# Performance work log

Measured on AMD Instinct MI355X. Metric: run time of the kernel, lower is better.

## Reference

```python
import jax, jax.numpy as jnp
import numpy as np

B, T, S, L, R, H, UE = 64, 256, 16, 128, 16, 256, 64


def setup_inputs() -> dict:
    key = jax.random.key(0)
    ks = jax.random.split(key, 10)
    u = jax.random.normal(ks[0], (B, T, UE), jnp.float32)
    k = 0.1 * jax.random.normal(ks[1], (B, T, L), jnp.float32)
    K = 0.1 * jax.random.normal(ks[2], (B, T, L, R), jnp.float32)
    eps_z = jax.random.normal(ks[3], (T, S, B, L), jnp.float32)
    eps_w = jax.random.normal(ks[4], (T, S, B, R), jnp.float32)
    W1 = jax.random.normal(ks[5], (L, H), jnp.float32) / np.sqrt(L).astype(np.float32)
    W2 = jax.random.normal(ks[6], (H, L), jnp.float32) / np.sqrt(H).astype(np.float32)
    m_init = jax.random.normal(ks[7], (L,), jnp.float32)
    Q_diag = jax.random.uniform(ks[8], (L,), jnp.float32, 0.1, 1.0)
    Q0_diag = jax.random.uniform(ks[9], (L,), jnp.float32, 0.5, 1.5)
    return dict(u=u, k=k, K=K, eps_z=eps_z, eps_w=eps_w, W1=W1, W2=W2,
                m_init=m_init, Q_diag=Q_diag, Q0_diag=Q0_diag, n_samples=S)


def reference(u, k, K, eps_z, eps_w, W1, W2, m_init, Q_diag, Q0_diag, n_samples):
    Bn, Tn, Ln, Rn = K.shape
    ue = u.shape[-1]
    I_r = jnp.eye(Rn, dtype=K.dtype)

    def bmv(A, x):      # A: [B,L,R], x: [...,B,R] -> [...,B,L]
        return jnp.einsum('blr,...br->...bl', A, x)

    def bmvT(A, x):     # A: [B,L,R], x: [...,B,L] -> [...,B,R]
        return jnp.einsum('blr,...bl->...br', A, x)

    def mean_fn(z):
        return z + jnp.tanh(z @ W1) @ W2

    def step_core(m, K_t, k_t, ez, ew, q_a):
        # A = I + K^T diag(q_a) K  (rank x rank)
        A = I_r + jnp.einsum('blr,l,blq->brq', K_t, q_a, K_t)
        Lc = jnp.linalg.cholesky(A)
        Linv = jax.scipy.linalg.solve_triangular(
            Lc, jnp.broadcast_to(I_r, Lc.shape), lower=True)

        def csolve(x):  # solve A y = x via Linv^T Linv x
            y = jnp.einsum('bij,...bj->...bi', Linv, x)
            return jnp.einsum('bji,...bj->...bi', Linv, y)

        # gain direction; inner shift always uses Q_diag (as in torch source)
        g = k_t - bmv(K_t, csolve(bmvT(K_t, m + Q_diag * k_t)))
        m_f = m + q_a * g
        z_p = jnp.sqrt(q_a) * ez
        z_f = m_f + z_p - bmv(K_t, csolve(bmvT(K_t, z_p) + ew))
        qp = jnp.sum(q_a * g * g, axis=-1)
        M = A - I_r  # = K^T diag(q_a) K
        tr = -jnp.einsum('bij,bjk,bik->b', Linv, M, Linv)
        logdet = 2.0 * jnp.sum(jnp.log(jnp.diagonal(Lc, axis1=-2, axis2=-1)), axis=-1)
        kl = 0.5 * (qp + tr + logdet)
        return z_f, m_f, z_p, kl

    # ---- t = 0 (uses initial covariance Q0_diag) ----
    m0 = jnp.broadcast_to(m_init, (Bn, Ln))
    m0 = m0.at[:, :ue].add(u[:, 0])
    z_f0, m_f0, z_p0, kl0 = step_core(m0, K[:, 0], k[:, 0], eps_z[0], eps_w[0], Q0_diag)

    # ---- t = 1..T-1: sequential nonlinear filter scan ----
    def scan_fn(z_prev, xs):
        u_t, k_t, K_t, ez, ew = xs
        m = mean_fn(z_prev)            # [S,B,L]
        m = m.at[..., :ue].add(u_t)    # broadcast input over samples
        z_f, m_f, z_p, kl = step_core(m, K_t, k_t, ez, ew, Q_diag)
        return z_f, (z_f, m_f.mean(axis=0), z_p, kl.mean(axis=0))

    xs = (jnp.swapaxes(u[:, 1:], 0, 1),
          jnp.swapaxes(k[:, 1:], 0, 1),
          jnp.swapaxes(K[:, 1:], 0, 1),
          eps_z[1:], eps_w[1:])
    _, (z_fs, m_fs, z_ps, kls) = jax.lax.scan(scan_fn, z_f0, xs)

    z_f = jnp.transpose(jnp.concatenate([z_f0[None], z_fs], 0), (1, 2, 0, 3))  # [S,B,T,L]
    m_f = jnp.transpose(jnp.concatenate([m_f0[None], m_fs], 0), (1, 0, 2))     # [B,T,L]
    z_p = jnp.transpose(jnp.concatenate([z_p0[None], z_ps], 0), (1, 2, 0, 3))  # [S,B,T,L]
    kl = jnp.concatenate([kl0[None], kls], 0).T                                 # [B,T]
    return z_f, m_f, z_p, kl
```

## Files before the change

### kernel.cpp

```cpp
#include <hip/hip_runtime.h>
#include <cstddef>

typedef _Float16 half8v __attribute__((ext_vector_type(8)));
typedef _Float16 half4v __attribute__((ext_vector_type(4)));
typedef float f32x4 __attribute__((ext_vector_type(4)));

#define MFMA32(A, B, C) __builtin_amdgcn_mfma_f32_16x16x32_f16(A, B, C, 0, 0, 0)
#define MFMA16(A, B, C) __builtin_amdgcn_mfma_f32_16x16x16f16(A, B, C, 0, 0, 0)

__global__ void kw2_kernel(const float* __restrict__ W2, _Float16* __restrict__ w2h) {
  int i = blockIdx.x * 256 + threadIdx.x;
  w2h[i] = (_Float16)W2[i];
}

__global__ void kprep1_kernel(const float* __restrict__ Kg,
                              const float* __restrict__ kg,
                              const float* __restrict__ ug,
                              const float* __restrict__ Qd,
                              const float* __restrict__ Q0d,
                              float* __restrict__ Ainv,
                              float* __restrict__ klc,
                              _Float16* __restrict__ pfb,
                              float* __restrict__ cgp) {
  int tid = threadIdx.x;
  int wv = tid >> 6, ln = tid & 63;
  size_t bt = (size_t)blockIdx.x * 4 + wv;
  int t = (int)(bt & 255);
  __shared__ float Ks[4][128][20];
  __shared__ float qs[4][128];
  __shared__ float vvs[4][128];
  __shared__ float Asm[4][16][20];
  __shared__ float LiL[4][16][20];
  __shared__ float AiS[4][16][20];
  __shared__ float yps[4][4][16];
  __shared__ float yvs[4][16];

  const float* kp = Kg + bt * 2048;
  for (int i = ln; i < 2048; i += 64) Ks[wv][i >> 4][i & 15] = kp[i];
  for (int l = ln; l < 128; l += 64) {
    float q = (t == 0) ? Q0d[l] : Qd[l];
    qs[wv][l] = q;
    float v = Qd[l] * kg[bt * 128 + l];
    if (t > 0 && l < 64) v += ug[bt * 64 + l];
    vvs[wv][l] = v;
  }
  __syncthreads();
  {
    int r = ln & 15, c0 = (ln >> 4) << 2;
    float a0 = 0, a1 = 0, a2 = 0, a3 = 0;
    for (int l = 0; l < 128; ++l) {
      float kq = Ks[wv][l][r] * qs[wv][l];
      const float* row = &Ks[wv][l][c0];
      a0 += kq * row[0]; a1 += kq * row[1]; a2 += kq * row[2]; a3 += kq * row[3];
    }
    Asm[wv][r][c0 + 0] = a0 + ((r == c0 + 0) ? 1.f : 0.f);
    Asm[wv][r][c0 + 1] = a1 + ((r == c0 + 1) ? 1.f : 0.f);
    Asm[wv][r][c0 + 2] = a2 + ((r == c0 + 2) ? 1.f : 0.f);
    Asm[wv][r][c0 + 3] = a3 + ((r == c0 + 3) ? 1.f : 0.f);
  }
  {
    int r = ln & 15, seg = ln >> 4;
    float s = 0.f;
    for (int l = seg * 32; l < seg * 32 + 32; ++l) s += Ks[wv][l][r] * vvs[wv][l];
    yps[wv][seg][r] = s;
  }
  __syncthreads();
  if (ln < 16) {
    int i = ln;
    float ar[16], Lr[16];
#pragma unroll
    for (int j = 0; j < 16; ++j) ar[j] = Asm[wv][i][j];
    float ld = 0.f;
#pragma unroll
    for (int j = 0; j < 16; ++j) {
      float ajj = __shfl(ar[j], j, 64);
      float d = sqrtf(ajj);
      ld += __logf(d);
      float li = ar[j] / d;
      li = (i >= j) ? li : 0.f;
      Lr[j] = li;
#pragma unroll
      for (int k2 = j; k2 < 16; ++k2) {
        float lk = __shfl(li, k2, 64);
        ar[k2] -= li * lk;
      }
    }
    int cc = i;
    float Lic[16];
#pragma unroll
    for (int ii = 0; ii < 16; ++ii) {
      float s = (ii == cc) ? 1.f : 0.f;
#pragma unroll
      for (int p = 0; p < 16; ++p) {
        if (p < ii) {
          float Lip = __shfl(Lr[p], ii, 64);
          s -= Lip * Lic[p];
        }
      }
      float dii = __shfl(Lr[ii], ii, 64);
      float v = s / dii;
      Lic[ii] = (ii >= cc) ? v : 0.f;
    }
    float tr = 0.f;
#pragma unroll
    for (int ii = 0; ii < 16; ++ii) { tr += Lic[ii] * Lic[ii]; LiL[wv][cc][ii] = Lic[ii]; }
    tr += __shfl_xor(tr, 1); tr += __shfl_xor(tr, 2);
    tr += __shfl_xor(tr, 4); tr += __shfl_xor(tr, 8);
    if (cc == 0) klc[bt] = 0.5f * (tr - 16.f + 2.f * ld);
    yvs[wv][cc] = yps[wv][0][cc] + yps[wv][1][cc] + yps[wv][2][cc] + yps[wv][3][cc];
  }
  __syncthreads();
  {
    int r = ln & 15, c0 = (ln >> 4) << 2;
    float a0 = 0, a1 = 0, a2 = 0, a3 = 0;
    for (int ii = 0; ii < 16; ++ii) {
      float lir = LiL[wv][r][ii];
      a0 += lir * LiL[wv][c0 + 0][ii];
      a1 += lir * LiL[wv][c0 + 1][ii];
      a2 += lir * LiL[wv][c0 + 2][ii];
      a3 += lir * LiL[wv][c0 + 3][ii];
    }
    AiS[wv][r][c0 + 0] = a0; AiS[wv][r][c0 + 1] = a1;
    AiS[wv][r][c0 + 2] = a2; AiS[wv][r][c0 + 3] = a3;
    f32x4 av = {a0, a1, a2, a3};
    *(f32x4*)&Ainv[bt * 256 + r * 16 + c0] = av;
  }
  __syncthreads();
  {
#pragma unroll
    for (int li = 0; li < 2; ++li) {
      int l = ln * 2 + li;
      f32x4 acc0 = {0,0,0,0}, acc1v = {0,0,0,0}, acc2v = {0,0,0,0}, acc3v = {0,0,0,0};
      for (int j = 0; j < 16; ++j) {
        float kj = Ks[wv][l][j];
        acc0  += kj * *(const f32x4*)&AiS[wv][j][0];
        acc1v += kj * *(const f32x4*)&AiS[wv][j][4];
        acc2v += kj * *(const f32x4*)&AiS[wv][j][8];
        acc3v += kj * *(const f32x4*)&AiS[wv][j][12];
      }
      float ql = qs[wv][l];
      float cp = ql * kg[bt * 128 + l];
      float pv[16];
#pragma unroll
      for (int e = 0; e < 4; ++e) {
        pv[e] = ql * acc0[e]; pv[4 + e] = ql * acc1v[e];
        pv[8 + e] = ql * acc2v[e]; pv[12 + e] = ql * acc3v[e];
      }
#pragma unroll
      for (int r = 0; r < 16; ++r) cp -= pv[r] * yvs[wv][r];
      cgp[bt * 128 + l] = cp;
#pragma unroll
      for (int r = 0; r < 16; ++r) Ks[wv][l][r] = pv[r];
    }
  }
  __syncthreads();
  {
    int gp = ln >> 4, cp = ln & 15;
#pragma unroll
    for (int ci = 0; ci < 4; ++ci) {
      half8v o;
#pragma unroll
      for (int mt = 0; mt < 2; ++mt)
#pragma unroll
        for (int j = 0; j < 4; ++j)
          o[mt * 4 + j] = (_Float16)Ks[wv][ci * 32 + mt * 16 + cp][gp * 4 + j];
      *(half8v*)(pfb + bt * 2048 + (size_t)(ci * 64 + ln) * 8) = o;
    }
  }
}

__global__ void kprepR_kernel(const float* __restrict__ Kg,
                              const _Float16* __restrict__ w2h,
                              _Float16* __restrict__ rfb,
                              _Float16* __restrict__ kab) {
  int tid = threadIdx.x;
  int wv = tid >> 6, ln = tid & 63;
  int g = ln >> 4, c = ln & 15;
  __shared__ _Float16 Kh[128][20];
  __shared__ _Float16 Rh[16][264];
  for (int it = 0; it < 4; ++it) {
    size_t bt = (size_t)blockIdx.x * 4 + it;
    const float* kp = Kg + bt * 2048;
    for (int i = tid; i < 2048; i += 256) Kh[i >> 4][i & 15] = (_Float16)kp[i];
    __syncthreads();
    half8v kA[4];
#pragma unroll
    for (int kt = 0; kt < 4; ++kt)
#pragma unroll
      for (int j = 0; j < 8; ++j) kA[kt][j] = Kh[kt * 32 + g * 8 + j][c];
#pragma unroll
    for (int i = 0; i < 4; ++i) {
      int tile = wv * 4 + i;
      f32x4 acc = {0, 0, 0, 0};
#pragma unroll
      for (int kt = 0; kt < 4; ++kt) {
        half8v bf = *(const half8v*)&w2h[(size_t)(tile * 16 + c) * 128 + kt * 32 + g * 8];
        acc = MFMA32(kA[kt], bf, acc);
      }
#pragma unroll
      for (int r = 0; r < 4; ++r) Rh[g * 4 + r][tile * 16 + c] = (_Float16)acc[r];
    }
    __syncthreads();
    half8v r0, r1;
#pragma unroll
    for (int mt = 0; mt < 4; ++mt)
#pragma unroll
      for (int j = 0; j < 4; ++j) {
        _Float16 v = Rh[c][wv * 64 + mt * 16 + g * 4 + j];
        if (mt < 2) r0[mt * 4 + j] = v; else r1[(mt - 2) * 4 + j] = v;
      }
    *(half8v*)(rfb + bt * 4096 + (size_t)tid * 16) = r0;
    *(half8v*)(rfb + bt * 4096 + (size_t)tid * 16 + 8) = r1;
    if (kab) {
      half8v ko;
#pragma unroll
      for (int kt = 0; kt < 2; ++kt)
#pragma unroll
        for (int j = 0; j < 4; ++j) ko[kt * 4 + j] = Kh[wv * 32 + kt * 16 + g * 4 + j][c];
      *(half8v*)(kab + bt * 2048 + (size_t)tid * 8) = ko;
    }
    __syncthreads();
  }
}

__global__ void kc_kernel(const float* __restrict__ Kg,
                          const float* __restrict__ epsz,
                          const float* __restrict__ epsw,
                          const float* __restrict__ Qd,
                          const float* __restrict__ Q0d,
                          const float* __restrict__ Ainv,
                          float* __restrict__ out_zf,
                          float* __restrict__ out_zp,
                          float* __restrict__ zpcb,
                          int zw, int wzp) {
  int idx = blockIdx.x;
  int t = idx >> 6, b = idx & 63;
  int bt = b * 256 + t;
  __shared__ float Ks[128][16];
  __shared__ float Ai[16][16];
  __shared__ float zp[16][129];
  __shared__ float hh[16][17];
  __shared__ float ww[16][17];
  __shared__ float sq[128];
  const float* kp = Kg + (size_t)bt * 2048;
  for (int i = threadIdx.x; i < 2048; i += 256) ((float*)Ks)[i] = kp[i];
  ((float*)Ai)[threadIdx.x] = Ainv[(size_t)bt * 256 + threadIdx.x];
  const float* q = (t == 0) ? Q0d : Qd;
  if (threadIdx.x < 128) sq[threadIdx.x] = sqrtf(q[threadIdx.x]);
  __syncthreads();
  for (int i = threadIdx.x; i < 2048; i += 256) {
    int s = i >> 7, l = i & 127;
    float v = sq[l] * epsz[(((size_t)t * 16 + s) * 64 + b) * 128 + l];
    zp[s][l] = v;
    if (wzp) out_zp[(((size_t)s * 64 + b) * 256 + t) * 128 + l] = v;
  }
  __syncthreads();
  {
    int s = threadIdx.x >> 4, r = threadIdx.x & 15;
    float acc = epsw[(((size_t)t * 16 + s) * 64 + b) * 16 + r];
    for (int l = 0; l < 128; ++l) acc += Ks[l][r] * zp[s][l];
    hh[s][r] = acc;
  }
  __syncthreads();
  {
    int s = threadIdx.x >> 4, r = threadIdx.x & 15;
    float acc = 0.f;
    for (int j = 0; j < 16; ++j) acc += Ai[r][j] * hh[s][j];
    ww[s][r] = acc;
  }
  __syncthreads();
  for (int i = threadIdx.x; i < 2048; i += 256) {
    int s = i >> 7, l = i & 127;
    float acc = 0.f;
    for (int r = 0; r < 16; ++r) acc += Ks[l][r] * ww[s][r];
    float v = zp[s][l] - acc;
    if (zw) zpcb[(size_t)bt * 2048 + i] = v;
    else out_zf[(((size_t)s * 64 + b) * 256 + t) * 128 + l] = v;
  }
}

__global__ void kzp_kernel(const float* __restrict__ epsz,
                           const float* __restrict__ Qd,
                           const float* __restrict__ Q0d,
                           float* __restrict__ out_zp) {
  for (size_t i = (size_t)blockIdx.x * blockDim.x + threadIdx.x; i < (size_t)33554432;
       i += (size_t)gridDim.x * blockDim.x) {
    int l = (int)(i & 127);
    int t = (int)((i >> 7) & 255);
    int sb = (int)(i >> 15);
    int s = sb >> 6, b = sb & 63;
    float q = (t == 0) ? Q0d[l] : Qd[l];
    out_zp[i] = sqrtf(q) * epsz[(((size_t)t * 16 + s) * 64 + b) * 128 + l];
  }
}

#define BAR() asm volatile("s_waitcnt lgkmcnt(0)\n\ts_barrier" ::: "memory")

template <bool PK, bool ZW>
__device__ __forceinline__ void scan_body(
    const int b, const int ct,
    _Float16* __restrict__ svhc, _Float16* __restrict__ hbc,
    float (*__restrict__ h2pc)[320], float (*__restrict__ qppc)[64],
    const float* __restrict__ ug, const float* __restrict__ Kg,
    const float* __restrict__ W1, const float* __restrict__ W2,
    const float* __restrict__ m_init, const float* __restrict__ Qd,
    const float* __restrict__ Q0d, const _Float16* __restrict__ pfb,
    const float* __restrict__ cgp, const _Float16* __restrict__ rfb,
    const _Float16* __restrict__ kab, const float* __restrict__ zpcb,
    const float* __restrict__ klcp, float* __restrict__ out_zf,
    float* __restrict__ out_mf, float* __restrict__ out_kl) {
  const int wvc = ct >> 6;
  const int ln = ct & 63;
  const int g = ln >> 4;
  const int c = ln & 15;

  half8v w1f[4][4];
#pragma unroll
  for (int mt = 0; mt < 4; ++mt)
#pragma unroll
    for (int kt = 0; kt < 4; ++kt) {
      half8v v;
#pragma unroll
      for (int j = 0; j < 8; ++j)
        v[j] = (_Float16)W1[(size_t)(kt * 32 + g * 8 + j) * 256 + (wvc * 64 + mt * 16 + c)];
      w1f[mt][kt] = v;
    }
  half8v w2f[2][8];
#pragma unroll
  for (int mt = 0; mt < 2; ++mt)
#pragma unroll
    for (int kt = 0; kt < 8; ++kt) {
      half8v v;
#pragma unroll
      for (int j = 0; j < 8; ++j)
        v[j] = (_Float16)W2[(size_t)(kt * 32 + g * 8 + j) * 128 + (wvc * 32 + mt * 16 + c)];
      w2f[mt][kt] = v;
    }

  f32x4 qiv[2], qiv0[2];
#pragma unroll
  for (int mt = 0; mt < 2; ++mt) {
    f32x4 q = *(const f32x4*)&Qd[wvc * 32 + mt * 16 + g * 4];
    f32x4 q0 = *(const f32x4*)&Q0d[wvc * 32 + mt * 16 + g * 4];
#pragma unroll
    for (int r = 0; r < 4; ++r) { qiv[mt][r] = 1.f / q[r]; qiv0[mt][r] = 1.f / q0[r]; }
  }

  f32x4 zreg[2];

  half8v pfx0, pfx1, kax0 = {}, kax1 = {}, rfa0, rfa1, rfc0, rfc1;
  float kf0[8], kf1[8];
  f32x4 zq0[2], zq1[2], cv0[2], cv1[2];
  f32x4 ur0[2] = {}, ur1[2] = {};
  float kv0 = 0.f, kv1 = 0.f;

  const char* pf_p = (const char*)pfb + (size_t)b * 256 * 4096 + (size_t)ct * 16;
  const char* ka_p = PK ? (const char*)kab + (size_t)b * 256 * 4096 + (size_t)ct * 16
                        : (const char*)pfb;
  const char* K_p = (const char*)Kg + (size_t)b * 256 * 8192 + (size_t)((wvc * 32 + g * 4) * 16 + c) * 4;
  const char* rf_p = (const char*)rfb + (size_t)b * 256 * 8192 + (size_t)ct * 32;
  const char* zq_p = ZW ? (const char*)zpcb + (size_t)b * 256 * 8192 + (size_t)(c * 128 + wvc * 32 + g * 4) * 4
                        : (const char*)out_zf + ((((size_t)c * 64 + b) * 256) * 128 + wvc * 32 + g * 4) * 4;
  const size_t zq_str = ZW ? 8192 : 512;
  const char* cv_p = (const char*)cgp + (size_t)b * 256 * 512 + (size_t)(wvc * 32 + g * 4) * 4;
  const char* ur_p = (const char*)ug + (size_t)b * 256 * 256 + (size_t)(wvc * 32 + g * 4) * 4;
  const char* kl_p = (const char*)klcp + (size_t)b * 256 * 4;
  char* zf_p = (char*)out_zf + ((((size_t)c * 64 + b) * 256) * 128 + wvc * 32 + g * 4) * 4;
  char* mf_p = (char*)out_mf + ((size_t)b * 256 * 128 + wvc * 32 + g * 4) * 4;

#define STAGE(BI) do { \
    pfx##BI = *(const half8v*)pf_p; pf_p += 4096; \
    if constexpr (PK) { kax##BI = *(const half8v*)ka_p; ka_p += 4096; } \
    else { _Pragma("unroll") for (int kt_ = 0; kt_ < 2; ++kt_) \
             _Pragma("unroll") for (int j_ = 0; j_ < 4; ++j_) \
               kf##BI[kt_ * 4 + j_] = *(const float*)(K_p + kt_ * 1024 + j_ * 64); \
           K_p += 8192; } \
    rfa##BI = *(const half8v*)rf_p; rfc##BI = *(const half8v*)(rf_p + 16); rf_p += 8192; \
    zq##BI[0] = *(const f32x4*)zq_p; zq##BI[1] = *(const f32x4*)(zq_p + 64); zq_p += zq_str; \
    cv##BI[0] = *(const f32x4*)cv_p; cv##BI[1] = *(const f32x4*)(cv_p + 64); cv_p += 512; \
    if (wvc < 2) { ur##BI[0] = *(const f32x4*)ur_p; ur##BI[1] = *(const f32x4*)(ur_p + 64); } \
    ur_p += 256; \
    kv##BI = *(const float*)kl_p; kl_p += 4; \
  } while (0)

#define KAH(BI, KT, DST) do { \
    if constexpr (PK) { _Pragma("unroll") for (int j_ = 0; j_ < 4; ++j_) DST[j_] = kax##BI[(KT) * 4 + j_]; } \
    else { _Pragma("unroll") for (int j_ = 0; j_ < 4; ++j_) DST[j_] = (_Float16)kf##BI[(KT) * 4 + j_]; } \
  } while (0)

#define PHASE_A(BI) do { \
    half4v zbh_[2], zbl_[2]; \
    _Pragma("unroll") for (int kt = 0; kt < 2; ++kt) \
      _Pragma("unroll") for (int j = 0; j < 4; ++j) { \
        float x_ = zreg[kt][j]; _Float16 h_ = (_Float16)x_; \
        zbh_[kt][j] = h_; zbl_[kt][j] = (_Float16)(x_ - (float)h_); } \
    half8v zh8_[4]; \
    _Pragma("unroll") for (int kt = 0; kt < 4; ++kt) { \
      int row_ = kt * 4 + g; \
      int idx_ = row_ * 128 + (((c + row_) & 15) << 3); \
      zh8_[kt] = *(const half8v*)&svhc[idx_]; } \
    f32x4 a1h_[4]; \
    _Pragma("unroll") for (int mt = 0; mt < 4; ++mt) a1h_[mt] = (f32x4){0,0,0,0}; \
    _Pragma("unroll") for (int kt = 0; kt < 4; ++kt) \
      _Pragma("unroll") for (int mt = 0; mt < 4; ++mt) \
        a1h_[mt] = MFMA32(w1f[mt][kt], zh8_[kt], a1h_[mt]); \
    half4v th_[4]; \
    _Pragma("unroll") for (int mt = 0; mt < 4; ++mt) { \
      _Pragma("unroll") for (int r = 0; r < 4; ++r) { \
        float x_ = a1h_[mt][r]; \
        float e_ = __expf(2.f * x_); \
        th_[mt][r] = (_Float16)(1.f - 2.f / (e_ + 1.f)); } \
      int row_ = wvc * 8 + mt * 2 + (g >> 1); \
      *(half4v*)&hbc[row_ * 128 + (((c + row_) & 15) << 3) + ((g & 1) << 2)] = th_[mt]; } \
    half4v ka0_, ka1_; KAH(BI, 0, ka0_); KAH(BI, 1, ka1_); \
    f32x4 hz_ = {0, 0, 0, 0}; \
    hz_ = MFMA16(ka0_, zbh_[0], hz_); hz_ = MFMA16(ka1_, zbh_[1], hz_); \
    hz_ = MFMA16(ka0_, zbl_[0], hz_); hz_ = MFMA16(ka1_, zbl_[1], hz_); \
    f32x4 hr_ = {0, 0, 0, 0}; \
    _Pragma("unroll") for (int mt = 0; mt < 4; ++mt) { \
      half4v rr_; \
      _Pragma("unroll") for (int j = 0; j < 4; ++j) \
        rr_[j] = (mt < 2) ? rfa##BI[mt * 4 + j] : rfc##BI[(mt - 2) * 4 + j]; \
      hr_ = MFMA16(rr_, th_[mt], hr_); } \
    *(f32x4*)&h2pc[wvc][c * 20 + g * 4] = hz_ + hr_; \
  } while (0)

#define EPILOG(BI, QIV, MV) do { \
    f32x4 h2v_ = *(const f32x4*)&h2pc[0][c * 20 + g * 4]; \
    h2v_ += *(const f32x4*)&h2pc[1][c * 20 + g * 4]; \
    h2v_ += *(const f32x4*)&h2pc[2][c * 20 + g * 4]; \
    h2v_ += *(const f32x4*)&h2pc[3][c * 20 + g * 4]; \
    half4v h2h_, h2l_; \
    _Pragma("unroll") for (int j = 0; j < 4; ++j) { \
      _Float16 h_ = (_Float16)h2v_[j]; \
      h2h_[j] = h_; h2l_[j] = (_Float16)(h2v_[j] - (float)h_); } \
    float qpl_ = 0.f; \
    _Pragma("unroll") for (int mt = 0; mt < 2; ++mt) { \
      half4v pfm_; \
      _Pragma("unroll") for (int j = 0; j < 4; ++j) pfm_[j] = pfx##BI[mt * 4 + j]; \
      f32x4 zz_ = {0, 0, 0, 0}; \
      f32x4 mh_ = MFMA16(pfm_, h2h_, zz_); \
      f32x4 mlv_ = MFMA16(pfm_, h2l_, zz_); \
      f32x4 dd_ = cv##BI[mt] - (mh_ + mlv_); \
      f32x4 mf_ = MV[mt] + dd_; \
      f32x4 zf_ = mf_ + zq##BI[mt]; \
      _Pragma("unroll") for (int r = 0; r < 4; ++r) qpl_ += dd_[r] * dd_[r] * QIV[mt][r]; \
      *(f32x4*)(zf_p + mt * 64) = zf_; \
      zreg[mt] = zf_; \
      half4v zh4_; \
      _Pragma("unroll") for (int r = 0; r < 4; ++r) zh4_[r] = (_Float16)zf_[r]; \
      int row_ = wvc * 4 + mt * 2 + (g >> 1); \
      int base_ = row_ * 128 + (((c + row_) & 15) << 3) + ((g & 1) << 2); \
      *(half4v*)&svhc[base_] = zh4_; \
      f32x4 ms_ = mf_; \
      _Pragma("unroll") for (int r = 0; r < 4; ++r) { \
        float x_ = ms_[r]; \
        x_ += __shfl_xor(x_, 1); x_ += __shfl_xor(x_, 2); \
        x_ += __shfl_xor(x_, 4); x_ += __shfl_xor(x_, 8); \
        ms_[r] = x_ * 0.0625f; } \
      if (c == 0) *(f32x4*)(mf_p + mt * 64) = ms_; \
    } \
    zf_p += 512; mf_p += 512; \
    qpl_ += __shfl_xor(qpl_, 16); \
    qpl_ += __shfl_xor(qpl_, 32); \
    if (g == 0) qppc[BI][wvc * 16 + c] = qpl_; \
  } while (0)

#define PHASE_B(BI, QIV) do { \
    half8v hf_[8]; \
    _Pragma("unroll") for (int kt = 0; kt < 8; ++kt) { \
      int row_ = kt * 4 + g; \
      hf_[kt] = *(const half8v*)&hbc[row_ * 128 + (((c + row_) & 15) << 3)]; } \
    f32x4 a2a_[2], a2b_[2]; \
    _Pragma("unroll") for (int mt = 0; mt < 2; ++mt) { a2a_[mt] = (f32x4){0,0,0,0}; a2b_[mt] = (f32x4){0,0,0,0}; } \
    _Pragma("unroll") for (int kt = 0; kt < 4; ++kt) \
      _Pragma("unroll") for (int mt = 0; mt < 2; ++mt) { \
        a2a_[mt] = MFMA32(w2f[mt][kt], hf_[kt], a2a_[mt]); \
        a2b_[mt] = MFMA32(w2f[mt][kt + 4], hf_[kt + 4], a2b_[mt]); } \
    f32x4 mv_[2]; \
    _Pragma("unroll") for (int mt = 0; mt < 2; ++mt) { \
      mv_[mt] = zreg[mt] + a2a_[mt] + a2b_[mt]; \
      if (wvc < 2) mv_[mt] += ur##BI[mt]; } \
    EPILOG(BI, QIV, mv_); \
  } while (0)

#define KL_FIN(PBI, TPREV) do { \
    if (ct < 16) { \
      float v_ = qppc[PBI][ct] + qppc[PBI][16 + ct] + qppc[PBI][32 + ct] + qppc[PBI][48 + ct]; \
      v_ += __shfl_xor(v_, 1); v_ += __shfl_xor(v_, 2); \
      v_ += __shfl_xor(v_, 4); v_ += __shfl_xor(v_, 8); \
      if (ct == 0) out_kl[(size_t)b * 256 + (size_t)(TPREV)] = 0.03125f * v_ + kv##PBI; \
    } \
  } while (0)

  STAGE(0);
  STAGE(1);
  {
    f32x4 mv0[2];
#pragma unroll
    for (int mt = 0; mt < 2; ++mt) {
      mv0[mt] = *(const f32x4*)&m_init[wvc * 32 + mt * 16 + g * 4];
      if (wvc < 2) mv0[mt] += ur0[mt];
    }
    half4v mh0[2], ml0[2];
#pragma unroll
    for (int kt = 0; kt < 2; ++kt)
#pragma unroll
      for (int j = 0; j < 4; ++j) {
        float x = mv0[kt][j];
        _Float16 h = (_Float16)x;
        mh0[kt][j] = h;
        ml0[kt][j] = (_Float16)(x - (float)h);
      }
    half4v ka0_, ka1_;
    KAH(0, 0, ka0_); KAH(0, 1, ka1_);
    f32x4 hz = {0, 0, 0, 0};
    hz = MFMA16(ka0_, mh0[0], hz); hz = MFMA16(ka1_, mh0[1], hz);
    hz = MFMA16(ka0_, ml0[0], hz); hz = MFMA16(ka1_, ml0[1], hz);
    *(f32x4*)&h2pc[wvc][c * 20 + g * 4] = hz;
    BAR();
    EPILOG(0, qiv0, mv0);
    BAR();
  }

  for (int t = 1; t < 255; t += 2) {
    KL_FIN(0, t - 1);
    STAGE(0);
    PHASE_A(1);
    BAR();
    PHASE_B(1, qiv);
    BAR();
    KL_FIN(1, t);
    STAGE(1);
    PHASE_A(0);
    BAR();
    PHASE_B(0, qiv);
    BAR();
  }
  KL_FIN(0, 254);
  PHASE_A(1);
  BAR();
  PHASE_B(1, qiv);
  BAR();
  KL_FIN(1, 255);

#undef STAGE
#undef KAH
#undef PHASE_A
#undef EPILOG
#undef PHASE_B
#undef KL_FIN
}

template <bool PK, bool ZW>
__launch_bounds__(256, 1)
__global__ void kscan1_kernel(const float* __restrict__ ug, const float* __restrict__ Kg,
                              const float* __restrict__ W1, const float* __restrict__ W2,
                              const float* __restrict__ m_init, const float* __restrict__ Qd,
                              const float* __restrict__ Q0d, const _Float16* __restrict__ pfb,
                              const float* __restrict__ cgp, const _Float16* __restrict__ rfb,
                              const _Float16* __restrict__ kab, const float* __restrict__ zpcb,
                              const float* __restrict__ klcp, float* __restrict__ out_zf,
                              float* __restrict__ out_mf, float* __restrict__ out_kl) {
  __shared__ __align__(16) _Float16 svh[2048];
  __shared__ __align__(16) _Float16 hb[4096];
  __shared__ float h2p[4][320];
  __shared__ float qpp[2][64];
  scan_body<PK, ZW>(blockIdx.x, threadIdx.x, svh, hb, h2p, qpp,
                    ug, Kg, W1, W2, m_init, Qd, Q0d, pfb, cgp, rfb, kab, zpcb, klcp,
                    out_zf, out_mf, out_kl);
}

template <bool PK, bool ZW>
__attribute__((amdgpu_flat_work_group_size(512, 512)))
__attribute__((amdgpu_waves_per_eu(2, 2)))
__global__ void kscan2_kernel(const float* __restrict__ ug, const float* __restrict__ Kg,
                              const float* __restrict__ W1, const float* __restrict__ W2,
                              const float* __restrict__ m_init, const float* __restrict__ Qd,
                              const float* __restrict__ Q0d, const _Float16* __restrict__ pfb,
                              const float* __restrict__ cgp, const _Float16* __restrict__ rfb,
                              const _Float16* __restrict__ kab, const float* __restrict__ zpcb,
                              const float* __restrict__ klcp, float* __restrict__ out_zf,
                              float* __restrict__ out_mf, float* __restrict__ out_kl) {
  __shared__ __align__(16) _Float16 svh[2][2048];
  __shared__ __align__(16) _Float16 hb[2][4096];
  __shared__ float h2p[2][4][320];
  __shared__ float qpp[2][2][64];
  const int ch = threadIdx.x >> 8;
  scan_body<PK, ZW>(blockIdx.x * 2 + ch, threadIdx.x & 255,
                    svh[ch], hb[ch], h2p[ch], qpp[ch],
                    ug, Kg, W1, W2, m_init, Qd, Q0d, pfb, cgp, rfb, kab, zpcb, klcp,
                    out_zf, out_mf, out_kl);
}

extern "C" void kernel_launch(void* const* d_in, const int* in_sizes, int n_in,
                              void* d_out, int out_size, void* d_ws, size_t ws_size,
                              hipStream_t stream) {
  (void)in_sizes; (void)n_in; (void)out_size;
  const float* u   = (const float*)d_in[0];
  const float* kk  = (const float*)d_in[1];
  const float* Kg  = (const float*)d_in[2];
  const float* epz = (const float*)d_in[3];
  const float* epw = (const float*)d_in[4];
  const float* W1  = (const float*)d_in[5];
  const float* W2  = (const float*)d_in[6];
  const float* mi  = (const float*)d_in[7];
  const float* Qd  = (const float*)d_in[8];
  const float* Q0d = (const float*)d_in[9];

  float* out_zf = (float*)d_out;
  float* out_mf = out_zf + (size_t)33554432;
  float* out_zp = out_mf + (size_t)2097152;
  float* out_kl = out_zp + (size_t)33554432;

  char* ws = (char*)d_ws;
  size_t off = 0;
  auto take = [&](size_t n) { char* p = ws + off; off += n; return p; };
  float*    Ainv = (float*)take(16777216);
  float*    klc  = (float*)take(65536);
  float*    cgp  = (float*)take(8388608);
  _Float16* pfb  = (_Float16*)take(67108864);
  _Float16* w2h  = (_Float16*)take(65536);
  bool zw = ws_size >= off + 134217728;
  float* zpcb = zw ? (float*)take(134217728) : nullptr;
  bool pk = zw && (ws_size >= off + 67108864);
  _Float16* kab = pk ? (_Float16*)take(67108864) : nullptr;
  bool rfws = ws_size >= off + 134217728;
  _Float16* rfb = rfws ? (_Float16*)take(134217728) : (_Float16*)out_zp;
  int wzp = rfws ? 1 : 0;

  kw2_kernel<<<128, 256, 0, stream>>>(W2, w2h);
  kprep1_kernel<<<4096, 256, 0, stream>>>(Kg, kk, u, Qd, Q0d, Ainv, klc, pfb, cgp);
  kprepR_kernel<<<4096, 256, 0, stream>>>(Kg, w2h, rfb, kab);
  kc_kernel<<<16384, 256, 0, stream>>>(Kg, epz, epw, Qd, Q0d, Ainv, out_zf, out_zp,
                                       zpcb, zw ? 1 : 0, wzp);

  auto pick = [&](const void* f2) {
    hipFuncAttributes fa;
    if (hipFuncGetAttributes(&fa, f2) == hipSuccess)
      return fa.localSizeBytes == 0 && fa.numRegs > 140;
    return false;
  };
#define LAUNCH_SCAN(PKV, ZWV) do { \
    if (pick((const void*)kscan2_kernel<PKV, ZWV>)) \
      kscan2_kernel<PKV, ZWV><<<32, 512, 0, stream>>>(u, Kg, W1, W2, mi, Qd, Q0d, pfb, cgp, rfb, kab, zpcb, klc, out_zf, out_mf, out_kl); \
    else \
      kscan1_kernel<PKV, ZWV><<<64, 256, 0, stream>>>(u, Kg, W1, W2, mi, Qd, Q0d, pfb, cgp, rfb, kab, zpcb, klc, out_zf, out_mf, out_kl); \
  } while (0)

  if (pk)      LAUNCH_SCAN(true,  true);
  else if (zw) LAUNCH_SCAN(false, true);
  else         LAUNCH_SCAN(false, false);
#undef LAUNCH_SCAN

  if (!rfws) kzp_kernel<<<2048, 256, 0, stream>>>(epz, Qd, Q0d, out_zp);
}
```

Baseline: 1.078 ms.

## Interleave two batch chains per 256-thread block in scan kernel

Replaces the 512-thread two-chain scan kernel with a 256-thread kernel in which each wave processes two independent batch elements (A and B), interleaving their phases so one chain's MFMA and memory latency can hide behind the other's. W1/W2 fragments are held in registers across both chains, and the launch picker now only requires zero scratch spills. This gives more instruction-level parallelism per wave at the cost of much higher register pressure, and it uses half as many waves per block.

```diff
diff --git a/kernel.cpp b/kernel.cpp
--- a/kernel.cpp
+++ b/kernel.cpp
@@ -572,9 +572,8 @@
 }
 
 template <bool PK, bool ZW>
-__attribute__((amdgpu_flat_work_group_size(512, 512)))
-__attribute__((amdgpu_waves_per_eu(2, 2)))
-__global__ void kscan2_kernel(const float* __restrict__ ug, const float* __restrict__ Kg,
+__launch_bounds__(256, 1)
+__global__ void kscand_kernel(const float* __restrict__ ug, const float* __restrict__ Kg,
                               const float* __restrict__ W1, const float* __restrict__ W2,
                               const float* __restrict__ m_init, const float* __restrict__ Qd,
                               const float* __restrict__ Q0d, const _Float16* __restrict__ pfb,
@@ -582,15 +581,293 @@
                               const _Float16* __restrict__ kab, const float* __restrict__ zpcb,
                               const float* __restrict__ klcp, float* __restrict__ out_zf,
                               float* __restrict__ out_mf, float* __restrict__ out_kl) {
+  const int tid = threadIdx.x;
+  const int wvc = tid >> 6;
+  const int ln = tid & 63;
+  const int g = ln >> 4;
+  const int c = ln & 15;
+  const int bA = blockIdx.x * 2;
+  const int bB = bA + 1;
+
   __shared__ __align__(16) _Float16 svh[2][2048];
   __shared__ __align__(16) _Float16 hb[2][4096];
   __shared__ float h2p[2][4][320];
   __shared__ float qpp[2][2][64];
-  const int ch = threadIdx.x >> 8;
-  scan_body<PK, ZW>(blockIdx.x * 2 + ch, threadIdx.x & 255,
-                    svh[ch], hb[ch], h2p[ch], qpp[ch],
-                    ug, Kg, W1, W2, m_init, Qd, Q0d, pfb, cgp, rfb, kab, zpcb, klcp,
-                    out_zf, out_mf, out_kl);
+
+  half8v w1f[4][4];
+#pragma unroll
+  for (int mt = 0; mt < 4; ++mt)
+#pragma unroll
+    for (int kt = 0; kt < 4; ++kt) {
+      half8v v;
+#pragma unroll
+      for (int j = 0; j < 8; ++j)
+        v[j] = (_Float16)W1[(size_t)(kt * 32 + g * 8 + j) * 256 + (wvc * 64 + mt * 16 + c)];
+      w1f[mt][kt] = v;
+    }
+  half8v w2f[2][8];
+#pragma unroll
+  for (int mt = 0; mt < 2; ++mt)
+#pragma unroll
+    for (int kt = 0; kt < 8; ++kt) {
+      half8v v;
+#pragma unroll
+      for (int j = 0; j < 8; ++j)
+        v[j] = (_Float16)W2[(size_t)(kt * 32 + g * 8 + j) * 128 + (wvc * 32 + mt * 16 + c)];
+      w2f[mt][kt] = v;
+    }
+
+  f32x4 qiv[2];
+#pragma unroll
+  for (int mt = 0; mt < 2; ++mt) {
+    f32x4 q = *(const f32x4*)&Qd[wvc * 32 + mt * 16 + g * 4];
+#pragma unroll
+    for (int r = 0; r < 4; ++r) qiv[mt][r] = 1.f / q[r];
+  }
+
+  f32x4 zregA[2], zregB[2];
+  half8v pfxA, pfxB, kaxA = {}, kaxB = {}, rfaA, rfaB, rfcA, rfcB;
+  float kfA[8], kfB[8];
+  f32x4 zqA[2], zqB[2], cvA[2], cvB[2], urA[2] = {}, urB[2] = {};
+  float kvA = 0.f, kvB = 0.f;
+
+  const int lo16 = tid * 16;
+  const int lo32 = tid * 32;
+  const int loK = ((wvc * 32 + g * 4) * 16 + c) * 4;
+  const int lodim = (wvc * 32 + g * 4) * 4;
+  const size_t zqlane = (size_t)(c * 128 + wvc * 32 + g * 4) * 4;
+  const size_t zflane = (size_t)c * 8388608 + (size_t)lodim;
+
+#define DSTAGE1(CH, BT) do { \
+    size_t o_ = (size_t)(BT); \
+    pfx##CH = *(const half8v*)((const char*)pfb + o_ * 4096 + lo16); \
+    if constexpr (PK) { kax##CH = *(const half8v*)((const char*)kab + o_ * 4096 + lo16); } \
+    else { _Pragma("unroll") for (int kt_ = 0; kt_ < 2; ++kt_) \
+             _Pragma("unroll") for (int j_ = 0; j_ < 4; ++j_) \
+               kf##CH[kt_ * 4 + j_] = *(const float*)((const char*)Kg + o_ * 8192 + loK + kt_ * 1024 + j_ * 64); } \
+    rfa##CH = *(const half8v*)((const char*)rfb + o_ * 8192 + lo32); \
+    rfc##CH = *(const half8v*)((const char*)rfb + o_ * 8192 + lo32 + 16); \
+  } while (0)
+
+#define DSTAGE2(CH, B_, BT, T) do { \
+    size_t o_ = (size_t)(BT); \
+    if constexpr (ZW) { \
+      zq##CH[0] = *(const f32x4*)((const char*)zpcb + o_ * 8192 + zqlane); \
+      zq##CH[1] = *(const f32x4*)((const char*)zpcb + o_ * 8192 + zqlane + 64); \
+    } else { \
+      size_t zo_ = (size_t)(B_) * 131072 + (size_t)(T) * 512 + zflane; \
+      zq##CH[0] = *(const f32x4*)((const char*)out_zf + zo_); \
+      zq##CH[1] = *(const f32x4*)((const char*)out_zf + zo_ + 64); \
+    } \
+    cv##CH[0] = *(const f32x4*)((const char*)cgp + o_ * 512 + lodim); \
+    cv##CH[1] = *(const f32x4*)((const char*)cgp + o_ * 512 + lodim + 64); \
+    if (wvc < 2) { \
+      ur##CH[0] = *(const f32x4*)((const char*)ug + o_ * 256 + lodim); \
+      ur##CH[1] = *(const f32x4*)((const char*)ug + o_ * 256 + lodim + 64); \
+    } \
+    kv##CH = klcp[BT]; \
+  } while (0)
+
+#define DKAH(CH, KT, DST) do { \
+    if constexpr (PK) { _Pragma("unroll") for (int j_ = 0; j_ < 4; ++j_) DST[j_] = kax##CH[(KT) * 4 + j_]; } \
+    else { _Pragma("unroll") for (int j_ = 0; j_ < 4; ++j_) DST[j_] = (_Float16)kf##CH[(KT) * 4 + j_]; } \
+  } while (0)
+
+#define DPHA(CH, CHI) do { \
+    half4v zbh_[2], zbl_[2]; \
+    _Pragma("unroll") for (int kt = 0; kt < 2; ++kt) \
+      _Pragma("unroll") for (int j = 0; j < 4; ++j) { \
+        float x_ = zreg##CH[kt][j]; _Float16 h_ = (_Float16)x_; \
+        zbh_[kt][j] = h_; zbl_[kt][j] = (_Float16)(x_ - (float)h_); } \
+    half8v zh8_[4]; \
+    _Pragma("unroll") for (int kt = 0; kt < 4; ++kt) { \
+      int row_ = kt * 4 + g; \
+      zh8_[kt] = *(const half8v*)&svh[CHI][row_ * 128 + (((c + row_) & 15) << 3)]; } \
+    f32x4 a1a_[4], a1b_[4]; \
+    _Pragma("unroll") for (int mt = 0; mt < 4; ++mt) { a1a_[mt] = (f32x4){0,0,0,0}; a1b_[mt] = (f32x4){0,0,0,0}; } \
+    _Pragma("unroll") for (int mt = 0; mt < 4; ++mt) { \
+      a1a_[mt] = MFMA32(w1f[mt][0], zh8_[0], a1a_[mt]); \
+      a1a_[mt] = MFMA32(w1f[mt][1], zh8_[1], a1a_[mt]); \
+      a1b_[mt] = MFMA32(w1f[mt][2], zh8_[2], a1b_[mt]); \
+      a1b_[mt] = MFMA32(w1f[mt][3], zh8_[3], a1b_[mt]); } \
+    half4v th_[4]; \
+    _Pragma("unroll") for (int mt = 0; mt < 4; ++mt) { \
+      _Pragma("unroll") for (int r = 0; r < 4; ++r) { \
+        float x_ = a1a_[mt][r] + a1b_[mt][r]; \
+        float e_ = __expf(2.f * x_); \
+        th_[mt][r] = (_Float16)(1.f - 2.f / (e_ + 1.f)); } \
+      int row_ = wvc * 8 + mt * 2 + (g >> 1); \
+      *(half4v*)&hb[CHI][row_ * 128 + (((c + row_) & 15) << 3) + ((g & 1) << 2)] = th_[mt]; } \
+    half4v ka0_, ka1_; DKAH(CH, 0, ka0_); DKAH(CH, 1, ka1_); \
+    f32x4 hz_ = {0, 0, 0, 0}; \
+    hz_ = MFMA16(ka0_, zbh_[0], hz_); hz_ = MFMA16(ka1_, zbh_[1], hz_); \
+    hz_ = MFMA16(ka0_, zbl_[0], hz_); hz_ = MFMA16(ka1_, zbl_[1], hz_); \
+    f32x4 hr_ = {0, 0, 0, 0}; \
+    _Pragma("unroll") for (int mt = 0; mt < 4; ++mt) { \
+      half4v rr_; \
+      _Pragma("unroll") for (int j = 0; j < 4; ++j) \
+        rr_[j] = (mt < 2) ? rfa##CH[mt * 4 + j] : rfc##CH[(mt - 2) * 4 + j]; \
+      hr_ = MFMA16(rr_, th_[mt], hr_); } \
+    *(f32x4*)&h2p[CHI][wvc][c * 20 + g * 4] = hz_ + hr_; \
+  } while (0)
+
+#define DEPI(CH, CHI, B_, T, QIV, MV) do { \
+    f32x4 h2v_ = *(const f32x4*)&h2p[CHI][0][c * 20 + g * 4]; \
+    h2v_ += *(const f32x4*)&h2p[CHI][1][c * 20 + g * 4]; \
+    h2v_ += *(const f32x4*)&h2p[CHI][2][c * 20 + g * 4]; \
+    h2v_ += *(const f32x4*)&h2p[CHI][3][c * 20 + g * 4]; \
+    half4v h2h_, h2l_; \
+    _Pragma("unroll") for (int j = 0; j < 4; ++j) { \
+      _Float16 h_ = (_Float16)h2v_[j]; \
+      h2h_[j] = h_; h2l_[j] = (_Float16)(h2v_[j] - (float)h_); } \
+    float qpl_ = 0.f; \
+    _Pragma("unroll") for (int mt = 0; mt < 2; ++mt) { \
+      half4v pfm_; \
+      _Pragma("unroll") for (int j = 0; j < 4; ++j) pfm_[j] = pfx##CH[mt * 4 + j]; \
+      f32x4 zz_ = {0, 0, 0, 0}; \
+      f32x4 mh_ = MFMA16(pfm_, h2h_, zz_); \
+      f32x4 mlv_ = MFMA16(pfm_, h2l_, zz_); \
+      f32x4 dd_ = cv##CH[mt] - (mh_ + mlv_); \
+      f32x4 mf_ = MV[mt] + dd_; \
+      f32x4 zf_ = mf_ + zq##CH[mt]; \
+      _Pragma("unroll") for (int r = 0; r < 4; ++r) qpl_ += dd_[r] * dd_[r] * QIV[mt][r]; \
+      *(f32x4*)((char*)out_zf + (size_t)(B_) * 131072 + (size_t)(T) * 512 + zflane + mt * 64) = zf_; \
+      zreg##CH[mt] = zf_; \
+      half4v zh4_; \
+      _Pragma("unroll") for (int r = 0; r < 4; ++r) zh4_[r] = (_Float16)zf_[r]; \
+      int row_ = wvc * 4 + mt * 2 + (g >> 1); \
+      *(half4v*)&svh[CHI][row_ * 128 + (((c + row_) & 15) << 3) + ((g & 1) << 2)] = zh4_; \
+      f32x4 ms_ = mf_; \
+      _Pragma("unroll") for (int r = 0; r < 4; ++r) { \
+        float x_ = ms_[r]; \
+        x_ += __shfl_xor(x_, 1); x_ += __shfl_xor(x_, 2); \
+        x_ += __shfl_xor(x_, 4); x_ += __shfl_xor(x_, 8); \
+        ms_[r] = x_ * 0.0625f; } \
+      if (c == 0) \
+        *(f32x4*)((char*)out_mf + ((size_t)(B_) * 256 + (size_t)(T)) * 512 + lodim + mt * 64) = ms_; \
+    } \
+    qpl_ += __shfl_xor(qpl_, 16); \
+    qpl_ += __shfl_xor(qpl_, 32); \
+    if (g == 0) qpp[CHI][(T) & 1][wvc * 16 + c] = qpl_; \
+  } while (0)
+
+#define DPHB(CH, CHI, B_, T, QIV) do { \
+    half8v hfa_[4]; \
+    _Pragma("unroll") for (int kt = 0; kt < 4; ++kt) { \
+      int row_ = kt * 4 + g; \
+      hfa_[kt] = *(const half8v*)&hb[CHI][row_ * 128 + (((c + row_) & 15) << 3)]; } \
+    f32x4 a2a_[2]; \
+    a2a_[0] = (f32x4){0,0,0,0}; a2a_[1] = (f32x4){0,0,0,0}; \
+    _Pragma("unroll") for (int kt = 0; kt < 4; ++kt) \
+      _Pragma("unroll") for (int mt = 0; mt < 2; ++mt) \
+        a2a_[mt] = MFMA32(w2f[mt][kt], hfa_[kt], a2a_[mt]); \
+    half8v hfb_[4]; \
+    _Pragma("unroll") for (int kt = 0; kt < 4; ++kt) { \
+      int row_ = (kt + 4) * 4 + g; \
+      hfb_[kt] = *(const half8v*)&hb[CHI][row_ * 128 + (((c + row_) & 15) << 3)]; } \
+    f32x4 a2b_[2]; \
+    a2b_[0] = (f32x4){0,0,0,0}; a2b_[1] = (f32x4){0,0,0,0}; \
+    _Pragma("unroll") for (int kt = 0; kt < 4; ++kt) \
+      _Pragma("unroll") for (int mt = 0; mt < 2; ++mt) \
+        a2b_[mt] = MFMA32(w2f[mt][kt + 4], hfb_[kt], a2b_[mt]); \
+    f32x4 mv_[2]; \
+    _Pragma("unroll") for (int mt = 0; mt < 2; ++mt) { \
+      mv_[mt] = zreg##CH[mt] + a2a_[mt] + a2b_[mt]; \
+      if (wvc < 2) mv_[mt] += ur##CH[mt]; } \
+    DEPI(CH, CHI, B_, T, QIV, mv_); \
+  } while (0)
+
+#define DKL(CH, CHI, B_, TPREV) do { \
+    if (tid < 16) { \
+      const float* qq_ = qpp[CHI][(TPREV) & 1]; \
+      float v_ = qq_[tid] + qq_[16 + tid] + qq_[32 + tid] + qq_[48 + tid]; \
+      v_ += __shfl_xor(v_, 1); v_ += __shfl_xor(v_, 2); \
+      v_ += __shfl_xor(v_, 4); v_ += __shfl_xor(v_, 8); \
+      if (tid == 0) out_kl[(size_t)(B_) * 256 + (size_t)(TPREV)] = 0.03125f * v_ + kv##CH; \
+    } \
+  } while (0)
+
+  {
+    int btA = bA * 256, btB = bB * 256;
+    DSTAGE1(A, btA); DSTAGE1(B, btB);
+    DSTAGE2(A, bA, btA, 0); DSTAGE2(B, bB, btB, 0);
+    f32x4 qiv0[2];
+#pragma unroll
+    for (int mt = 0; mt < 2; ++mt) {
+      f32x4 q0 = *(const f32x4*)&Q0d[wvc * 32 + mt * 16 + g * 4];
+#pragma unroll
+      for (int r = 0; r < 4; ++r) qiv0[mt][r] = 1.f / q0[r];
+    }
+    f32x4 mvA_[2], mvB_[2];
+#pragma unroll
+    for (int mt = 0; mt < 2; ++mt) {
+      f32x4 mi = *(const f32x4*)&m_init[wvc * 32 + mt * 16 + g * 4];
+      mvA_[mt] = mi; mvB_[mt] = mi;
+      if (wvc < 2) { mvA_[mt] += urA[mt]; mvB_[mt] += urB[mt]; }
+    }
+    {
+      half4v mh0[2], ml0[2];
+#pragma unroll
+      for (int kt = 0; kt < 2; ++kt)
+#pragma unroll
+        for (int j = 0; j < 4; ++j) {
+          float x = mvA_[kt][j];
+          _Float16 h = (_Float16)x;
+          mh0[kt][j] = h; ml0[kt][j] = (_Float16)(x - (float)h);
+        }
+      half4v ka0_, ka1_;
+      DKAH(A, 0, ka0_); DKAH(A, 1, ka1_);
+      f32x4 hz = {0, 0, 0, 0};
+      hz = MFMA16(ka0_, mh0[0], hz); hz = MFMA16(ka1_, mh0[1], hz);
+      hz = MFMA16(ka0_, ml0[0], hz); hz = MFMA16(ka1_, ml0[1], hz);
+      *(f32x4*)&h2p[0][wvc][c * 20 + g * 4] = hz;
+    }
+    {
+      half4v mh0[2], ml0[2];
+#pragma unroll
+      for (int kt = 0; kt < 2; ++kt)
+#pragma unroll
+        for (int j = 0; j < 4; ++j) {
+          float x = mvB_[kt][j];
+          _Float16 h = (_Float16)x;
+          mh0[kt][j] = h; ml0[kt][j] = (_Float16)(x - (float)h);
+        }
+      half4v ka0_, ka1_;
+      DKAH(B, 0, ka0_); DKAH(B, 1, ka1_);
+      f32x4 hz = {0, 0, 0, 0};
+      hz = MFMA16(ka0_, mh0[0], hz); hz = MFMA16(ka1_, mh0[1], hz);
+      hz = MFMA16(ka0_, ml0[0], hz); hz = MFMA16(ka1_, ml0[1], hz);
+      *(f32x4*)&h2p[1][wvc][c * 20 + g * 4] = hz;
+    }
+    BAR();
+    DEPI(A, 0, bA, 0, qiv0, mvA_);
+    DEPI(B, 1, bB, 0, qiv0, mvB_);
+    BAR();
+  }
+
+  for (int t = 1; t < 256; ++t) {
+    DKL(A, 0, bA, t - 1);
+    DKL(B, 1, bB, t - 1);
+    int btA = bA * 256 + t, btB = bB * 256 + t;
+    DSTAGE1(A, btA); DSTAGE1(B, btB);
+    DPHA(A, 0);
+    DPHA(B, 1);
+    BAR();
+    DSTAGE2(A, bA, btA, t); DSTAGE2(B, bB, btB, t);
+    DPHB(A, 0, bA, t, qiv);
+    DPHB(B, 1, bB, t, qiv);
+    BAR();
+  }
+  DKL(A, 0, bA, 255);
+  DKL(B, 1, bB, 255);
+
+#undef DSTAGE1
+#undef DSTAGE2
+#undef DKAH
+#undef DPHA
+#undef DEPI
+#undef DPHB
+#undef DKL
 }
 
 extern "C" void kernel_launch(void* const* d_in, const int* in_sizes, int n_in,
@@ -635,15 +912,14 @@
   kc_kernel<<<16384, 256, 0, stream>>>(Kg, epz, epw, Qd, Q0d, Ainv, out_zf, out_zp,
                                        zpcb, zw ? 1 : 0, wzp);
 
-  auto pick = [&](const void* f2) {
+  auto ok = [&](const void* f) {
     hipFuncAttributes fa;
-    if (hipFuncGetAttributes(&fa, f2) == hipSuccess)
-      return fa.localSizeBytes == 0 && fa.numRegs > 140;
+    if (hipFuncGetAttributes(&fa, f) == hipSuccess) return fa.localSizeBytes == 0;
     return false;
   };
 #define LAUNCH_SCAN(PKV, ZWV) do { \
-    if (pick((const void*)kscan2_kernel<PKV, ZWV>)) \
-      kscan2_kernel<PKV, ZWV><<<32, 512, 0, stream>>>(u, Kg, W1, W2, mi, Qd, Q0d, pfb, cgp, rfb, kab, zpcb, klc, out_zf, out_mf, out_kl); \
+    if (ok((const void*)kscand_kernel<PKV, ZWV>)) \
+      kscand_kernel<PKV, ZWV><<<32, 256, 0, stream>>>(u, Kg, W1, W2, mi, Qd, Q0d, pfb, cgp, rfb, kab, zpcb, klc, out_zf, out_mf, out_kl); \
     else \
       kscan1_kernel<PKV, ZWV><<<64, 256, 0, stream>>>(u, Kg, W1, W2, mi, Qd, Q0d, pfb, cgp, rfb, kab, zpcb, klc, out_zf, out_mf, out_kl); \
   } while (0)
```

Result: slower. 1.850 ms (+71.6%).
